# Kernel tuning notes

Measured on AMD Instinct MI355X. Metric: run time of the kernel, lower is better.

## Reference

```python
import jax, jax.numpy as jnp
import numpy as np

B, S, D = 2, 2048, 1024
H = 16
HD = D // H  # 64
EPS = 1e-5


def setup_inputs() -> dict:
    key = jax.random.key(0)
    ks = jax.random.split(key, 9)
    s = 1.0 / np.sqrt(D)
    return {
        "x": jax.random.normal(ks[0], (B, S, D), jnp.float32),
        "Wq": jax.random.normal(ks[1], (D, D), jnp.float32) * s,
        "bq": jnp.zeros((D,), jnp.float32),
        "Wk": jax.random.normal(ks[2], (D, D), jnp.float32) * s,
        "bk": jnp.zeros((D,), jnp.float32),
        "Wv": jax.random.normal(ks[3], (D, D), jnp.float32) * s,
        "bv": jnp.zeros((D,), jnp.float32),
        "Wp": jax.random.normal(ks[4], (D, D), jnp.float32) * s,
        "bp": jnp.zeros((D,), jnp.float32),
        "gamma": jnp.ones((D,), jnp.float32),
        "beta": jnp.zeros((D,), jnp.float32),
    }


def reference(x, Wq, bq, Wk, bk, Wv, bv, Wp, bp, gamma, beta):
    # QKV projections -> [B, H, S, HD]
    def split_heads(t):
        return t.reshape(B, S, H, HD).transpose(0, 2, 1, 3)

    q = split_heads(x @ Wq + bq)
    k = split_heads(x @ Wk + bk)
    v = split_heads(x @ Wv + bv)

    scores = jnp.einsum('bhqd,bhkd->bhqk', q, k) / np.sqrt(HD).astype(jnp.float32)
    attn = jax.nn.softmax(scores, axis=-1)  # dropout in eval mode = identity
    out = jnp.einsum('bhqk,bhkd->bhqd', attn, v)
    out = out.transpose(0, 2, 1, 3).reshape(B, S, D)
    out = out @ Wp + bp  # dropout identity

    # residual + LayerNorm over last dim
    y = x + out
    mu = jnp.mean(y, axis=-1, keepdims=True)
    var = jnp.mean((y - mu) ** 2, axis=-1, keepdims=True)
    return (y - mu) / jnp.sqrt(var + EPS) * gamma + beta
```

## Files before the change

kernel.cpp:

```cpp
#include <hip/hip_runtime.h>

#define DI __device__ __forceinline__

typedef __bf16 bf16;
typedef __bf16 bf16x8 __attribute__((ext_vector_type(8)));
typedef __bf16 bf16x4 __attribute__((ext_vector_type(4)));
typedef float  f32x4  __attribute__((ext_vector_type(4)));

DI void async_copy16(const void* g, void* s) {
  __builtin_amdgcn_global_load_lds(
      (__attribute__((address_space(1))) unsigned int*)(void*)g,
      (__attribute__((address_space(3))) unsigned int*)s,
      16, 0, 0);
}

DI f32x4 mfma16(bf16x8 a, bf16x8 b, f32x4 c) {
  return __builtin_amdgcn_mfma_f32_16x16x32_bf16(a, b, c, 0, 0, 0);
}


__global__ __launch_bounds__(256) void convert_x(const float* __restrict__ x,
                                                 bf16* __restrict__ xb) {
  int t = blockIdx.x * 256 + threadIdx.x;
  float4 v = ((const float4*)x)[t];
  bf16x4 o;
  o[0] = (bf16)v.x; o[1] = (bf16)v.y; o[2] = (bf16)v.z; o[3] = (bf16)v.w;
  *(bf16x4*)&xb[t * 4] = o;
}

__global__ __launch_bounds__(256) void transpose_w(const float* __restrict__ Wq,
                                                   const float* __restrict__ Wk,
                                                   const float* __restrict__ Wv,
                                                   const float* __restrict__ Wp,
                                                   bf16* __restrict__ Wt) {
  __shared__ float tile[32][33];
  const float* W = (blockIdx.z == 0) ? Wq : (blockIdx.z == 1) ? Wk
                 : (blockIdx.z == 2) ? Wv : Wp;
  int n0 = blockIdx.x * 32, k0 = blockIdx.y * 32;
  int tx = threadIdx.x, ty = threadIdx.y;
#pragma unroll
  for (int i = 0; i < 4; ++i)
    tile[ty + i * 8][tx] = W[(k0 + ty + i * 8) * 1024 + n0 + tx];
  __syncthreads();
#pragma unroll
  for (int i = 0; i < 4; ++i)
    Wt[((int)blockIdx.z * 1024 + n0 + ty + i * 8) * 1024 + k0 + tx] =
        (bf16)tile[tx][ty + i * 8];
}

template <int MODE>
__global__ __launch_bounds__(256) void gemm_bt(
    const bf16* __restrict__ A, const bf16* __restrict__ Bt,
    const float* __restrict__ bias0, const float* __restrict__ bias1,
    const float* __restrict__ bias2, bf16* __restrict__ Qo,
    bf16* __restrict__ Ko, bf16* __restrict__ Vo, float* __restrict__ Po) {
  const int tid = threadIdx.x;
  const int w = tid >> 6, lane = tid & 63, quad = lane >> 4, m16 = lane & 15;
  const int m0 = blockIdx.x * 128, n0 = blockIdx.y * 128;
  const int mw = (w >> 1) * 64, nw = (w & 1) * 64;

  __shared__ __align__(16) bf16 As[128 * 32];
  __shared__ __align__(16) bf16 Bs[128 * 32];

  f32x4 acc[4][4];
#pragma unroll
  for (int i = 0; i < 4; ++i)
#pragma unroll
    for (int j = 0; j < 4; ++j)
#pragma unroll
      for (int r = 0; r < 4; ++r) acc[i][j][r] = 0.0f;

  for (int k0 = 0; k0 < 1024; k0 += 32) {
    __syncthreads();
#pragma unroll
    for (int i = 0; i < 2; ++i) {
      int lin = i * 256 + tid;
      int row = lin >> 2, col = (lin & 3) << 3;
      async_copy16(&A[(m0 + row) * 1024 + k0 + col], &As[(i * 256 + w * 64) * 8]);
      async_copy16(&Bt[(n0 + row) * 1024 + k0 + col], &Bs[(i * 256 + w * 64) * 8]);
    }
    __syncthreads();

    bf16x8 af[4], bg[4];
#pragma unroll
    for (int i = 0; i < 4; ++i) {
      af[i] = *(const bf16x8*)&As[(mw + i * 16 + m16) * 32 + quad * 8];
      bg[i] = *(const bf16x8*)&Bs[(nw + i * 16 + m16) * 32 + quad * 8];
    }
#pragma unroll
    for (int i = 0; i < 4; ++i)
#pragma unroll
      for (int j = 0; j < 4; ++j) acc[i][j] = mfma16(af[i], bg[j], acc[i][j]);
  }

  const float SC = 0.18033688011112042f;
#pragma unroll
  for (int i = 0; i < 4; ++i) {
#pragma unroll
    for (int j = 0; j < 4; ++j) {
      int np = n0 + nw + j * 16 + m16;
      if (MODE == 0) {
        int which = np >> 10, n = np & 1023;
        float bias = (which == 0) ? bias0[n] : (which == 1) ? bias1[n] : bias2[n];
        int h = n >> 6, hd = n & 63;
        if (which == 2) {
          bf16x4 pv;
          int m = m0 + mw + i * 16 + quad * 4;
          int b = m >> 11, s = m & 2047;
#pragma unroll
          for (int r = 0; r < 4; ++r) pv[r] = (bf16)(acc[i][j][r] + bias);
          *(bf16x4*)&Vo[((b * 16 + h) * 64 + hd) * 2048 + s] = pv;
        } else {
#pragma unroll
          for (int r = 0; r < 4; ++r) {
            int m = m0 + mw + i * 16 + quad * 4 + r;
            int b = m >> 11, s = m & 2047;
            float v = acc[i][j][r] + bias;
            if (which == 0)
              Qo[((b * 16 + h) * 2048 + s) * 64 + hd] = (bf16)(v * SC);
            else
              Ko[((b * 16 + h) * 2048 + s) * 64 + hd] = (bf16)v;
          }
        }
      } else {
        float bias = bias0[np];
#pragma unroll
        for (int r = 0; r < 4; ++r) {
          int m = m0 + mw + i * 16 + quad * 4 + r;
          Po[m * 1024 + np] = acc[i][j][r] + bias;
        }
      }
    }
  }
}

__global__ __launch_bounds__(256, 2) void flash_kernel(const bf16* __restrict__ Q,
                                                       const bf16* __restrict__ K,
                                                       const bf16* __restrict__ Vt,
                                                       bf16* __restrict__ attn) {
  const int S = 2048;
  const int tid = threadIdx.x;
  const int w = tid >> 6, lane = tid & 63, quad = lane >> 4, m16 = lane & 15;
  const int bh = blockIdx.y, b = bh >> 4, h = bh & 15;
  const int qb = blockIdx.x * 128;
  const bf16* Qh = Q + bh * S * 64;
  const bf16* Kh = K + bh * S * 64;
  const bf16* Vh = Vt + bh * 64 * S;

  __shared__ __align__(16) bf16 Ks[64 * 64];
  __shared__ __align__(16) bf16 Vs[64 * 64];
  __shared__ __align__(16) bf16 Ps[4][16 * 72];

  bf16x8 qf[2][2];
#pragma unroll
  for (int mi = 0; mi < 2; ++mi)
#pragma unroll
    for (int kk = 0; kk < 2; ++kk)
      qf[mi][kk] = *(const bf16x8*)&Qh[(qb + w * 32 + mi * 16 + m16) * 64 +
                                       kk * 32 + quad * 8];

  bf16x8 ones;
#pragma unroll
  for (int j = 0; j < 8; ++j) ones[j] = (bf16)1.0f;

  f32x4 o[2][4];
  f32x4 lacc[2];
#pragma unroll
  for (int mi = 0; mi < 2; ++mi) {
#pragma unroll
    for (int dt = 0; dt < 4; ++dt)
#pragma unroll
      for (int r = 0; r < 4; ++r) o[mi][dt][r] = 0.0f;
#pragma unroll
    for (int r = 0; r < 4; ++r) lacc[mi][r] = 0.0f;
  }

  for (int kb = 0; kb < S; kb += 64) {
    __syncthreads();
#pragma unroll
    for (int i = 0; i < 2; ++i) {
      int lin = i * 256 + tid;
      int row = lin >> 3, g = lin & 7;
      async_copy16(&Kh[(kb + row) * 64 + ((g ^ (row & 7)) << 3)],
                   &Ks[(i * 256 + w * 64) * 8]);
      async_copy16(&Vh[row * 2048 + kb + ((g ^ (row & 7)) << 3)],
                   &Vs[(i * 256 + w * 64) * 8]);
    }
    __syncthreads();

    bf16x8 kf[4][2], vf[4][2];
#pragma unroll
    for (int nt = 0; nt < 4; ++nt)
#pragma unroll
      for (int kk = 0; kk < 2; ++kk) {
        int row = nt * 16 + m16;
        int pos = (kk * 4 + quad) ^ (row & 7);
        kf[nt][kk] = *(const bf16x8*)&Ks[row * 64 + pos * 8];
        vf[nt][kk] = *(const bf16x8*)&Vs[row * 64 + pos * 8];
      }

    bf16* Pw = &Ps[w][0];
#pragma unroll
    for (int mi = 0; mi < 2; ++mi) {
      f32x4 sacc[4];
#pragma unroll
      for (int nt = 0; nt < 4; ++nt)
#pragma unroll
        for (int r = 0; r < 4; ++r) sacc[nt][r] = 0.0f;
#pragma unroll
      for (int nt = 0; nt < 4; ++nt)
#pragma unroll
        for (int kk = 0; kk < 2; ++kk)
          sacc[nt] = mfma16(kf[nt][kk], qf[mi][kk], sacc[nt]);

#pragma unroll
      for (int nt = 0; nt < 4; ++nt) {
        bf16x4 p4;
#pragma unroll
        for (int r = 0; r < 4; ++r)
          p4[r] = (bf16)__builtin_amdgcn_exp2f(sacc[nt][r]);
        *(bf16x4*)&Pw[m16 * 72 + nt * 16 + quad * 4] = p4;
      }
      asm volatile("s_waitcnt lgkmcnt(0)" ::: "memory");

      bf16x8 pf[2];
#pragma unroll
      for (int kk = 0; kk < 2; ++kk)
        pf[kk] = *(const bf16x8*)&Pw[m16 * 72 + kk * 32 + quad * 8];

#pragma unroll
      for (int kk = 0; kk < 2; ++kk) lacc[mi] = mfma16(pf[kk], ones, lacc[mi]);

#pragma unroll
      for (int dt = 0; dt < 4; ++dt)
#pragma unroll
        for (int kk = 0; kk < 2; ++kk)
          o[mi][dt] = mfma16(pf[kk], vf[dt][kk], o[mi][dt]);
    }
  }

#pragma unroll
  for (int mi = 0; mi < 2; ++mi) {
    f32x4 inv;
#pragma unroll
    for (int r = 0; r < 4; ++r) inv[r] = 1.0f / lacc[mi][r];
#pragma unroll
    for (int dt = 0; dt < 4; ++dt)
#pragma unroll
      for (int r = 0; r < 4; ++r) {
        int s = qb + w * 32 + mi * 16 + quad * 4 + r;
        int col = h * 64 + dt * 16 + m16;
        attn[(b * 2048 + s) * 1024 + col] = (bf16)(o[mi][dt][r] * inv[r]);
      }
  }
}

__global__ __launch_bounds__(256) void ln_kernel(const float* __restrict__ x,
                                                 const float* __restrict__ pj,
                                                 const float* __restrict__ gamma,
                                                 const float* __restrict__ beta,
                                                 float* __restrict__ out) {
  int row = blockIdx.x, t = threadIdx.x;
  int base = row * 1024 + t * 4;
  float4 xv = *(const float4*)&x[base];
  float4 pv = *(const float4*)&pj[base];
  float y0 = xv.x + pv.x, y1 = xv.y + pv.y, y2 = xv.z + pv.z, y3 = xv.w + pv.w;
  float s = y0 + y1 + y2 + y3;
  float ss = y0 * y0 + y1 * y1 + y2 * y2 + y3 * y3;
  for (int m = 1; m < 64; m <<= 1) {
    s += __shfl_xor(s, m);
    ss += __shfl_xor(ss, m);
  }
  __shared__ float sred[8];
  int w = t >> 6;
  if ((t & 63) == 0) { sred[w * 2] = s; sred[w * 2 + 1] = ss; }
  __syncthreads();
  s = sred[0] + sred[2] + sred[4] + sred[6];
  ss = sred[1] + sred[3] + sred[5] + sred[7];
  float mean = s * (1.0f / 1024.0f);
  float var = ss * (1.0f / 1024.0f) - mean * mean;
  float rstd = rsqrtf(var + 1e-5f);
  float4 gv = *(const float4*)&gamma[t * 4];
  float4 bv = *(const float4*)&beta[t * 4];
  float4 ov;
  ov.x = (y0 - mean) * rstd * gv.x + bv.x;
  ov.y = (y1 - mean) * rstd * gv.y + bv.y;
  ov.z = (y2 - mean) * rstd * gv.z + bv.z;
  ov.w = (y3 - mean) * rstd * gv.w + bv.w;
  *(float4*)&out[base] = ov;
}


extern "C" void kernel_launch(void* const* d_in, const int* in_sizes, int n_in,
                              void* d_out, int out_size, void* d_ws, size_t ws_size,
                              hipStream_t stream) {
  const float* x = (const float*)d_in[0];
  const float* Wq = (const float*)d_in[1];
  const float* bq = (const float*)d_in[2];
  const float* Wk = (const float*)d_in[3];
  const float* bk = (const float*)d_in[4];
  const float* Wv = (const float*)d_in[5];
  const float* bv = (const float*)d_in[6];
  const float* Wp = (const float*)d_in[7];
  const float* bp = (const float*)d_in[8];
  const float* gamma = (const float*)d_in[9];
  const float* beta = (const float*)d_in[10];
  float* out = (float*)d_out;

  char* ws = (char*)d_ws;
  bf16* xb = (bf16*)(ws);
  bf16* Wtb = (bf16*)(ws + (8u << 20));
  bf16* Qb = (bf16*)(ws + (16u << 20));
  bf16* Kb = (bf16*)(ws + (24u << 20));
  bf16* Vtb = (bf16*)(ws + (32u << 20));
  float* proj = (float*)(ws + (16u << 20));
  bf16* attn = xb;

  convert_x<<<4096, 256, 0, stream>>>(x, xb);
  transpose_w<<<dim3(32, 32, 4), dim3(32, 8), 0, stream>>>(Wq, Wk, Wv, Wp, Wtb);
  gemm_bt<0><<<dim3(32, 24), 256, 0, stream>>>(xb, Wtb, bq, bk, bv, Qb, Kb, Vtb,
                                               nullptr);
  flash_kernel<<<dim3(16, 32), 256, 0, stream>>>(Qb, Kb, Vtb, attn);
  gemm_bt<1><<<dim3(32, 8), 256, 0, stream>>>(attn, Wtb + 3072 * 1024, bp,
                                              nullptr, nullptr, nullptr, nullptr,
                                              nullptr, proj);
  ln_kernel<<<4096, 256, 0, stream>>>(x, proj, gamma, beta, out);
}
```

Baseline: 227.6 us.

## Template GEMM tiles, deepen K step to 64 with XOR-swizzled LDS, retile output projection

The GEMM kernel now takes its M/N tile sizes as template parameters and steps K by 64 per barrier pair instead of 32. Shared-memory rows are XOR-swizzled on load and read so the wider rows avoid LDS bank conflicts. The output projection switches to 64x128 tiles, doubling its grid to 512 blocks for better CU occupancy, and launch bounds request 3 waves per SIMD. The aim is fewer synchronizations per K and better GPU fill for the smaller GEMM, at the cost of more LDS per block.

```diff
diff --git a/kernel.cpp b/kernel.cpp
--- a/kernel.cpp
+++ b/kernel.cpp
@@ -48,56 +48,71 @@
         (bf16)tile[tx][ty + i * 8];
 }
 
-template <int MODE>
-__global__ __launch_bounds__(256) void gemm_bt(
+template <int MODE, int MT, int NT>
+__global__ __launch_bounds__(256, 3) void gemm_bt(
     const bf16* __restrict__ A, const bf16* __restrict__ Bt,
     const float* __restrict__ bias0, const float* __restrict__ bias1,
     const float* __restrict__ bias2, bf16* __restrict__ Qo,
     bf16* __restrict__ Ko, bf16* __restrict__ Vo, float* __restrict__ Po) {
+  constexpr int MW = MT / 2, NW = NT / 2;
+  constexpr int MI = MW / 16, NI = NW / 16;
   const int tid = threadIdx.x;
   const int w = tid >> 6, lane = tid & 63, quad = lane >> 4, m16 = lane & 15;
-  const int m0 = blockIdx.x * 128, n0 = blockIdx.y * 128;
-  const int mw = (w >> 1) * 64, nw = (w & 1) * 64;
-
-  __shared__ __align__(16) bf16 As[128 * 32];
-  __shared__ __align__(16) bf16 Bs[128 * 32];
-
-  f32x4 acc[4][4];
-#pragma unroll
-  for (int i = 0; i < 4; ++i)
-#pragma unroll
-    for (int j = 0; j < 4; ++j)
+  const int m0 = blockIdx.x * MT, n0 = blockIdx.y * NT;
+  const int mw = (w >> 1) * MW, nw = (w & 1) * NW;
+  const int sw = m16 & 7;
+
+  __shared__ __align__(16) bf16 As[MT * 64];
+  __shared__ __align__(16) bf16 Bs[NT * 64];
+
+  f32x4 acc[MI][NI];
+#pragma unroll
+  for (int i = 0; i < MI; ++i)
+#pragma unroll
+    for (int j = 0; j < NI; ++j)
 #pragma unroll
       for (int r = 0; r < 4; ++r) acc[i][j][r] = 0.0f;
 
-  for (int k0 = 0; k0 < 1024; k0 += 32) {
+  for (int k0 = 0; k0 < 1024; k0 += 64) {
     __syncthreads();
 #pragma unroll
-    for (int i = 0; i < 2; ++i) {
+    for (int i = 0; i < MT / 32; ++i) {
       int lin = i * 256 + tid;
-      int row = lin >> 2, col = (lin & 3) << 3;
-      async_copy16(&A[(m0 + row) * 1024 + k0 + col], &As[(i * 256 + w * 64) * 8]);
-      async_copy16(&Bt[(n0 + row) * 1024 + k0 + col], &Bs[(i * 256 + w * 64) * 8]);
+      int row = lin >> 3, p = lin & 7;
+      async_copy16(&A[(m0 + row) * 1024 + k0 + ((p ^ (row & 7)) << 3)],
+                   &As[(i * 256 + w * 64) * 8]);
+    }
+#pragma unroll
+    for (int i = 0; i < NT / 32; ++i) {
+      int lin = i * 256 + tid;
+      int row = lin >> 3, p = lin & 7;
+      async_copy16(&Bt[(n0 + row) * 1024 + k0 + ((p ^ (row & 7)) << 3)],
+                   &Bs[(i * 256 + w * 64) * 8]);
     }
     __syncthreads();
 
-    bf16x8 af[4], bg[4];
-#pragma unroll
-    for (int i = 0; i < 4; ++i) {
-      af[i] = *(const bf16x8*)&As[(mw + i * 16 + m16) * 32 + quad * 8];
-      bg[i] = *(const bf16x8*)&Bs[(nw + i * 16 + m16) * 32 + quad * 8];
-    }
-#pragma unroll
-    for (int i = 0; i < 4; ++i)
-#pragma unroll
-      for (int j = 0; j < 4; ++j) acc[i][j] = mfma16(af[i], bg[j], acc[i][j]);
+#pragma unroll
+    for (int kk = 0; kk < 2; ++kk) {
+      const int pos = ((kk * 4 + quad) ^ sw) << 3;
+      bf16x8 af[MI], bg[NI];
+#pragma unroll
+      for (int i = 0; i < MI; ++i)
+        af[i] = *(const bf16x8*)&As[(mw + i * 16 + m16) * 64 + pos];
+#pragma unroll
+      for (int j = 0; j < NI; ++j)
+        bg[j] = *(const bf16x8*)&Bs[(nw + j * 16 + m16) * 64 + pos];
+#pragma unroll
+      for (int i = 0; i < MI; ++i)
+#pragma unroll
+        for (int j = 0; j < NI; ++j) acc[i][j] = mfma16(af[i], bg[j], acc[i][j]);
+    }
   }
 
   const float SC = 0.18033688011112042f;
 #pragma unroll
-  for (int i = 0; i < 4; ++i) {
-#pragma unroll
-    for (int j = 0; j < 4; ++j) {
+  for (int i = 0; i < MI; ++i) {
+#pragma unroll
+    for (int j = 0; j < NI; ++j) {
       int np = n0 + nw + j * 16 + m16;
       if (MODE == 0) {
         int which = np >> 10, n = np & 1023;
@@ -318,11 +333,11 @@
 
   convert_x<<<4096, 256, 0, stream>>>(x, xb);
   transpose_w<<<dim3(32, 32, 4), dim3(32, 8), 0, stream>>>(Wq, Wk, Wv, Wp, Wtb);
-  gemm_bt<0><<<dim3(32, 24), 256, 0, stream>>>(xb, Wtb, bq, bk, bv, Qb, Kb, Vtb,
-                                               nullptr);
+  gemm_bt<0, 128, 128><<<dim3(32, 24), 256, 0, stream>>>(
+      xb, Wtb, bq, bk, bv, Qb, Kb, Vtb, nullptr);
   flash_kernel<<<dim3(16, 32), 256, 0, stream>>>(Qb, Kb, Vtb, attn);
-  gemm_bt<1><<<dim3(32, 8), 256, 0, stream>>>(attn, Wtb + 3072 * 1024, bp,
-                                              nullptr, nullptr, nullptr, nullptr,
-                                              nullptr, proj);
+  gemm_bt<1, 64, 128><<<dim3(64, 8), 256, 0, stream>>>(
+      attn, Wtb + 3072 * 1024, bp, nullptr, nullptr, nullptr, nullptr, nullptr,
+      proj);
   ln_kernel<<<4096, 256, 0, stream>>>(x, proj, gamma, beta, out);
 }
```

After: 195.2 us. 14.2% less time.
